# Performance work log

Measured on AMD Instinct MI355X. Metric: run time of the kernel, lower is better.

## Reference

```python
import jax, jax.numpy as jnp
import numpy as np

B, T, E, H = 8, 2048, 512, 16
D = E // H  # 32 embeddings per head
LN_EPS = 1e-3  # keras LayerNormalization default epsilon
DECAY = 1.2


def setup_inputs() -> dict:
    key = jax.random.key(0)
    k0, k1, k2 = jax.random.split(key, 3)
    x = jax.random.normal(k0, (B, T, E), dtype=jnp.float32)
    W = jax.random.normal(k1, (E, E), dtype=jnp.float32) * (1.0 / np.sqrt(E))
    b = jnp.zeros((E,), dtype=jnp.float32)
    concept_map = jax.random.normal(k2, (H, D, D, D), dtype=jnp.float32) * 0.02
    gamma = jnp.ones((E,), dtype=jnp.float32)
    beta = jnp.zeros((E,), dtype=jnp.float32)
    return {"x": x, "W": W, "b": b, "concept_map": concept_map,
            "gamma": gamma, "beta": beta}


def reference(x, W, b, concept_map, gamma, beta):
    Bn, Tn, En = x.shape
    Hn = concept_map.shape[0]
    Dn = En // Hn
    # Dense projection, split into heads: (B,T,H,D)
    h = (jnp.einsum('bte,ef->btf', x, W) + b).reshape(Bn, Tn, Hn, Dn)
    # Decayed cumulative sum of preceding tokens: S_0 = 0, S_t = (S_{t-1} + h_{t-1}) / 1.2
    def step(s, h_t):
        return (s + h_t) / DECAY, s
    _, S = jax.lax.scan(step, jnp.zeros((Bn, Hn, Dn), h.dtype),
                        jnp.swapaxes(h, 0, 1))  # S: (T,B,H,D)
    S = jnp.swapaxes(S, 0, 1)  # (B,T,H,D)
    # Fused bilinear contraction: sum_{i,j} h[...,i] * S[...,j] * C[h,k,i,j]
    # (equivalent to outer-product * concept_map then reduce_sum over last two dims)
    y = jnp.einsum('bthi,bthj,hkij->bthk', h, S, concept_map) + h
    y = y.reshape(Bn, Tn, En)
    # LayerNormalization over last axis (keras default eps=1e-3)
    mu = jnp.mean(y, axis=-1, keepdims=True)
    var = jnp.var(y, axis=-1, keepdims=True)
    y = (y - mu) * jax.lax.rsqrt(var + LN_EPS) * gamma + beta
    # Dropout: identity at inference
    return y
```

## Files before the change

### kernel.cpp

```cpp
#include <hip/hip_runtime.h>
#include <hip/hip_bf16.h>

#define Bn 8
#define Tn 2048
#define En 512
#define Hn 16
#define Dn 32
#define NC 32
#define CL 64
#define NT (Bn*Tn)
#define INV_DECAY (1.0f/1.2f)
#define LOG2_INVD (-0.26303440583379383f)

typedef __attribute__((ext_vector_type(8))) short  bf16x8;
typedef __attribute__((ext_vector_type(4))) float  f32x4;
typedef __attribute__((ext_vector_type(8))) unsigned short u16x8;

__device__ __forceinline__ unsigned short f2b(float f) {
    __hip_bfloat16 h = __float2bfloat16(f);
    return *reinterpret_cast<unsigned short*>(&h);
}
__device__ __forceinline__ float b2f(unsigned short u) {
    union { unsigned int i; float f; } c; c.i = ((unsigned int)u) << 16; return c.f;
}

__host__ __device__ constexpr float wpow(int e) {
    float r = 1.f;
    for (int i = 0; i < e; i++) r *= (1.0f / 1.2f);
    return r;
}

__device__ __forceinline__ size_t hm(int hd, int tok, int ch) {
    return (size_t)hd * ((size_t)NT * Dn) + (size_t)tok * Dn + ch;
}

__global__ __launch_bounds__(256) void prep_k(const float* __restrict__ C,
                                              unsigned short* __restrict__ Cl,
                                              const float* __restrict__ W,
                                              unsigned short* __restrict__ Wt) {
    __shared__ float tile[32][33];
    if (blockIdx.x < 256) {
        const int g = blockIdx.x * 256 + threadIdx.x;
        const int hd = g >> 12, rem = g & 4095;
        const int i = rem >> 7, half = (rem >> 6) & 1, lane = rem & 63;
        const int tloc = lane & 15, kgrp = lane >> 4;
        const int k = half * 16 + tloc;
        const float* src = C + (size_t)hd * 32768 + (size_t)k * 1024 + i * 32 + kgrp * 8;
        float4 a = reinterpret_cast<const float4*>(src)[0];
        float4 b = reinterpret_cast<const float4*>(src)[1];
        u16x8 st;
        st[0]=f2b(a.x); st[1]=f2b(a.y); st[2]=f2b(a.z); st[3]=f2b(a.w);
        st[4]=f2b(b.x); st[5]=f2b(b.y); st[6]=f2b(b.z); st[7]=f2b(b.w);
        *reinterpret_cast<u16x8*>(Cl + (size_t)g * 8) = st;
    } else {
        const int bid = blockIdx.x - 256;
        const int kb = (bid & 15) * 32, nb = (bid >> 4) * 32;
        const int tx = threadIdx.x & 31, ty = threadIdx.x >> 5;
        #pragma unroll
        for (int j = 0; j < 4; j++)
            tile[ty + 8 * j][tx] = W[(size_t)(kb + ty + 8 * j) * En + nb + tx];
        __syncthreads();
        #pragma unroll
        for (int j = 0; j < 4; j++)
            Wt[(size_t)(nb + ty + 8 * j) * En + kb + tx] = f2b(tile[tx][ty + 8 * j]);
    }
}

__global__ __launch_bounds__(256) void gemm_mfma_k(const float* __restrict__ x,
                                                   const unsigned short* __restrict__ Wt,
                                                   const float* __restrict__ bias,
                                                   unsigned short* __restrict__ h,
                                                   float* __restrict__ locals) {
    __shared__ unsigned short As[128][40];
    __shared__ unsigned short Bs[64][40];
    const int m0 = blockIdx.x * 128, n0 = blockIdx.y * 64;
    const int tid = threadIdx.x;
    const int wid = tid >> 6, lane = tid & 63;
    const int tloc = lane & 15, kgrp = lane >> 4;
    const int wr = wid >> 1, wc = wid & 1;

    const int ar = tid >> 1, ah = (tid & 1) * 16;
    const int brr = tid >> 2, bq = (tid & 3) * 8;

    f32x4 acc[4][2] = {};

    for (int k0 = 0; k0 < En; k0 += 32) {
        const float* xp = &x[(size_t)(m0 + ar) * En + k0 + ah];
        float4 a0 = reinterpret_cast<const float4*>(xp)[0];
        float4 a1 = reinterpret_cast<const float4*>(xp)[1];
        float4 a2 = reinterpret_cast<const float4*>(xp)[2];
        float4 a3 = reinterpret_cast<const float4*>(xp)[3];
        u16x8 bv = *reinterpret_cast<const u16x8*>(&Wt[(size_t)(n0 + brr) * En + k0 + bq]);
        __syncthreads();
        u16x8 w0, w1;
        w0[0]=f2b(a0.x); w0[1]=f2b(a0.y); w0[2]=f2b(a0.z); w0[3]=f2b(a0.w);
        w0[4]=f2b(a1.x); w0[5]=f2b(a1.y); w0[6]=f2b(a1.z); w0[7]=f2b(a1.w);
        w1[0]=f2b(a2.x); w1[1]=f2b(a2.y); w1[2]=f2b(a2.z); w1[3]=f2b(a2.w);
        w1[4]=f2b(a3.x); w1[5]=f2b(a3.y); w1[6]=f2b(a3.z); w1[7]=f2b(a3.w);
        *reinterpret_cast<u16x8*>(&As[ar][ah])     = w0;
        *reinterpret_cast<u16x8*>(&As[ar][ah + 8]) = w1;
        *reinterpret_cast<u16x8*>(&Bs[brr][bq])    = bv;
        __syncthreads();

        bf16x8 afr[4], bfr[2];
        #pragma unroll
        for (int m = 0; m < 4; m++)
            afr[m] = *reinterpret_cast<const bf16x8*>(&As[wr * 64 + m * 16 + tloc][kgrp * 8]);
        #pragma unroll
        for (int n = 0; n < 2; n++)
            bfr[n] = *reinterpret_cast<const bf16x8*>(&Bs[wc * 32 + n * 16 + tloc][kgrp * 8]);
        #pragma unroll
        for (int m = 0; m < 4; m++)
            #pragma unroll
            for (int n = 0; n < 2; n++)
                acc[m][n] = __builtin_amdgcn_mfma_f32_16x16x32_bf16(afr[m], bfr[n], acc[m][n], 0, 0, 0);
    }

    const float kmul = (kgrp & 1 ? 2.0736f : 1.f) * (kgrp & 2 ? 4.29981696f : 1.f);
    const int cg = blockIdx.x * 2 + wr;

    #pragma unroll
    for (int n = 0; n < 2; n++) {
        const int col = n0 + wc * 32 + n * 16 + tloc;
        const float bcol = bias[col];
        const int hd = col >> 5, ch = col & 31;
        float part = 0.f;
        #pragma unroll
        for (int m = 0; m < 4; m++)
            #pragma unroll
            for (int r = 0; r < 4; r++) {
                const int row = m0 + wr * 64 + m * 16 + kgrp * 4 + r;
                const unsigned short hb16 = f2b(acc[m][n][r] + bcol);
                h[hm(hd, row, ch)] = hb16;
                part += b2f(hb16) * (wpow(64 - m * 16 - r) * kmul);
            }
        part += __shfl_xor(part, 16);
        part += __shfl_xor(part, 32);
        if (kgrp == 0) locals[(size_t)cg * En + col] = part;
    }
}

__global__ __launch_bounds__(512) void scan_prefix_k(const float* __restrict__ locals,
                                                     float* __restrict__ Acar) {
    const int b = blockIdx.x;
    const int e = threadIdx.x;
    float invRL = 1.f;
    #pragma unroll
    for (int i = 0; i < CL; i++) invRL *= INV_DECAY;
    float A = 0.f;
    for (int c = 0; c < NC; c++) {
        Acar[(size_t)(b * NC + c) * En + e] = A;
        A = A * invRL + locals[(size_t)(b * NC + c) * En + e];
    }
}

__global__ __launch_bounds__(256, 2) void bilinear10_k(const unsigned short* __restrict__ hg,
                                                       const float* __restrict__ Acar,
                                                       unsigned short* __restrict__ yb,
                                                       const unsigned short* __restrict__ Cl) {
    __shared__ unsigned short hs[64][40];
    __shared__ unsigned short Ss[64][40];
    __shared__ float ys[4][64][33];

    const int hd = blockIdx.y;
    const int cg = blockIdx.x;
    const int tokens0 = cg * 64;
    const int tid = threadIdx.x;
    const int wid = tid >> 6, lane = tid & 63;
    const int tloc = lane & 15, kgrp = lane >> 4;
    const int j0 = kgrp * 8;
    const int c0 = wid * 8;

    bf16x8 afr[8][2];
    {
        const unsigned short* cb = Cl + (size_t)hd * 32768;
        #pragma unroll
        for (int s = 0; s < 8; s++) {
            const int i = wid * 8 + s;
            #pragma unroll
            for (int mt = 0; mt < 2; mt++)
                afr[s][mt] = *reinterpret_cast<const bf16x8*>(
                    cb + ((size_t)((i * 2 + mt) * 64 + lane) * 8));
        }
    }

    float Ac[8];
    #pragma unroll
    for (int e = 0; e < 8; e++)
        Ac[e] = Acar[(size_t)cg * En + hd * Dn + c0 + e];

    {
        const int tok = tid >> 2, c8 = (tid & 3) * 8;
        *reinterpret_cast<u16x8*>(&hs[tok][c8]) =
            *reinterpret_cast<const u16x8*>(hg + hm(hd, tokens0 + tok, c8));
    }
    __syncthreads();

    {
        float P[8];
        u16x8 hv = *reinterpret_cast<const u16x8*>(&hs[lane][c0]);
        #pragma unroll
        for (int e = 0; e < 8; e++) P[e] = b2f(hv[e]);
        #pragma unroll
        for (int k = 0; k < 6; k++) {
            const int dlt = 1 << k;
            const float wk = wpow(1 << k);
            #pragma unroll
            for (int e = 0; e < 8; e++) {
                float o = __shfl_up(P[e], dlt, 64);
                P[e] += (lane >= dlt) ? wk * o : 0.f;
            }
        }
        const float dt = exp2f((float)lane * LOG2_INVD);
        u16x8 sst;
        #pragma unroll
        for (int e = 0; e < 8; e++) {
            float pm1 = __shfl_up(P[e], 1, 64);
            if (lane == 0) pm1 = 0.f;
            sst[e] = f2b(Ac[e] * dt + INV_DECAY * pm1);
        }
        *reinterpret_cast<u16x8*>(&Ss[lane][c0]) = sst;
    }
    __syncthreads();

    u16x8 hreg[4];
    float sf[4][8];
    #pragma unroll
    for (int nt = 0; nt < 4; nt++) {
        const int trow = nt * 16 + tloc;
        hreg[nt] = *reinterpret_cast<const u16x8*>(&hs[trow][c0]);
        u16x8 sv = *reinterpret_cast<const u16x8*>(&Ss[trow][j0]);
        #pragma unroll
        for (int e = 0; e < 8; e++) sf[nt][e] = b2f(sv[e]);
    }

    f32x4 acc[2][4] = {};
    #pragma unroll
    for (int s = 0; s < 8; s++) {
        #pragma unroll
        for (int nt = 0; nt < 4; nt++) {
            const float hsc = b2f(hreg[nt][s]);
            bf16x8 bfrag;
            #pragma unroll
            for (int e = 0; e < 8; e++) bfrag[e] = (short)f2b(hsc * sf[nt][e]);
            acc[0][nt] = __builtin_amdgcn_mfma_f32_16x16x32_bf16(afr[s][0], bfrag, acc[0][nt], 0, 0, 0);
            acc[1][nt] = __builtin_amdgcn_mfma_f32_16x16x32_bf16(afr[s][1], bfrag, acc[1][nt], 0, 0, 0);
        }
    }

    #pragma unroll
    for (int mt = 0; mt < 2; mt++)
        #pragma unroll
        for (int nt = 0; nt < 4; nt++)
            #pragma unroll
            for (int r = 0; r < 4; r++)
                ys[wid][nt * 16 + tloc][mt * 16 + kgrp * 4 + r] = acc[mt][nt][r];
    __syncthreads();

    {
        const int token = tid >> 2, q = tid & 3;
        float y[8];
        #pragma unroll
        for (int e = 0; e < 8; e++) y[e] = 0.f;
        #pragma unroll
        for (int w = 0; w < 4; w++) {
            #pragma unroll
            for (int e = 0; e < 8; e++) y[e] += ys[w][token][q * 8 + e];
        }
        u16x8 hres = *reinterpret_cast<const u16x8*>(&hs[token][q * 8]);
        u16x8 st;
        #pragma unroll
        for (int e = 0; e < 8; e++) st[e] = f2b(y[e] + b2f(hres[e]));
        *reinterpret_cast<u16x8*>(yb + hm(hd, tokens0 + token, q * 8)) = st;
    }
}

__global__ __launch_bounds__(256) void ln_k(const unsigned short* __restrict__ y,
                                            const float* __restrict__ gamma,
                                            const float* __restrict__ beta,
                                            float* __restrict__ out) {
    const int row = blockIdx.x * 4 + (threadIdx.x >> 6);
    const int lane = threadIdx.x & 63;
    u16x8 v = *reinterpret_cast<const u16x8*>(y + hm(lane >> 2, row, (lane & 3) * 8));
    float f[8];
    float s = 0.f, s2 = 0.f;
    #pragma unroll
    for (int e = 0; e < 8; e++) {
        f[e] = b2f(v[e]);
        s += f[e]; s2 += f[e] * f[e];
    }
    #pragma unroll
    for (int off = 1; off < 64; off <<= 1) {
        s  += __shfl_xor(s, off);
        s2 += __shfl_xor(s2, off);
    }
    const float mu = s * (1.f / En);
    const float var = s2 * (1.f / En) - mu * mu;
    const float rs = rsqrtf(var + 1e-3f);
    const int cbase = lane * 8;
    float4 g0 = reinterpret_cast<const float4*>(&gamma[cbase])[0];
    float4 g1 = reinterpret_cast<const float4*>(&gamma[cbase])[1];
    float4 b0 = reinterpret_cast<const float4*>(&beta[cbase])[0];
    float4 b1 = reinterpret_cast<const float4*>(&beta[cbase])[1];
    float4 o0, o1;
    o0.x = (f[0] - mu) * rs * g0.x + b0.x; o0.y = (f[1] - mu) * rs * g0.y + b0.y;
    o0.z = (f[2] - mu) * rs * g0.z + b0.z; o0.w = (f[3] - mu) * rs * g0.w + b0.w;
    o1.x = (f[4] - mu) * rs * g1.x + b1.x; o1.y = (f[5] - mu) * rs * g1.y + b1.y;
    o1.z = (f[6] - mu) * rs * g1.z + b1.z; o1.w = (f[7] - mu) * rs * g1.w + b1.w;
    float* op = out + (size_t)row * En;
    reinterpret_cast<float4*>(op)[lane * 2]     = o0;
    reinterpret_cast<float4*>(op)[lane * 2 + 1] = o1;
}

extern "C" void kernel_launch(void* const* d_in, const int* in_sizes, int n_in,
                              void* d_out, int out_size, void* d_ws, size_t ws_size,
                              hipStream_t stream) {
    const float* x     = (const float*)d_in[0];
    const float* W     = (const float*)d_in[1];
    const float* bias  = (const float*)d_in[2];
    const float* C     = (const float*)d_in[3];
    const float* gamma = (const float*)d_in[4];
    const float* beta  = (const float*)d_in[5];
    float* out = (float*)d_out;

    unsigned short* hb  = (unsigned short*)d_ws;
    unsigned short* yb  = hb + (size_t)Hn * NT * Dn;
    unsigned short* Cl  = yb + (size_t)Hn * NT * Dn;
    unsigned short* Wt  = Cl + (size_t)Hn * Dn * Dn * Dn;
    float* locals = (float*)(Wt + (size_t)En * En);
    float* Acar   = locals + (size_t)Bn * NC * En;

    prep_k<<<512, 256, 0, stream>>>(C, Cl, W, Wt);
    gemm_mfma_k<<<dim3(NT / 128, En / 64), 256, 0, stream>>>(x, Wt, bias, hb, locals);
    scan_prefix_k<<<Bn, 512, 0, stream>>>(locals, Acar);
    bilinear10_k<<<dim3(NT / CL, Hn), 256, 0, stream>>>(hb, Acar, yb, Cl);
    ln_k<<<NT / 4, 256, 0, stream>>>(yb, gamma, beta, out);
}
```

Measured before the change: 81.80 us.

## Fuse chunk-carry prefix scan into bilinear kernel and halve cross-wave reduction buffer

Drops the separate scan_prefix_k launch. Each bilinear block now computes its own carry-in by summing the decayed locals of all preceding chunks in its batch, which means redundant work that grows with the chunk index. The cross-wave reduction now uses a smaller two-slot shared buffer with vectorized f32x4 accumulation, paying for it with an extra barrier. The launch-bounds occupancy hint is raised from 2 to 4, which may force register pressure or spills given the large afr fragment arrays.

New measurement: 104.0 us. 1.27x slower.

```diff
diff --git a/kernel.cpp b/kernel.cpp
--- a/kernel.cpp
+++ b/kernel.cpp
@@ -140,36 +140,24 @@
     }
 }
 
-__global__ __launch_bounds__(512) void scan_prefix_k(const float* __restrict__ locals,
-                                                     float* __restrict__ Acar) {
-    const int b = blockIdx.x;
-    const int e = threadIdx.x;
-    float invRL = 1.f;
-    #pragma unroll
-    for (int i = 0; i < CL; i++) invRL *= INV_DECAY;
-    float A = 0.f;
-    for (int c = 0; c < NC; c++) {
-        Acar[(size_t)(b * NC + c) * En + e] = A;
-        A = A * invRL + locals[(size_t)(b * NC + c) * En + e];
-    }
-}
-
-__global__ __launch_bounds__(256, 2) void bilinear10_k(const unsigned short* __restrict__ hg,
-                                                       const float* __restrict__ Acar,
+__global__ __launch_bounds__(256, 4) void bilinear13_k(const unsigned short* __restrict__ hg,
+                                                       const float* __restrict__ locals,
                                                        unsigned short* __restrict__ yb,
                                                        const unsigned short* __restrict__ Cl) {
     __shared__ unsigned short hs[64][40];
     __shared__ unsigned short Ss[64][40];
-    __shared__ float ys[4][64][33];
+    __shared__ float ys2[2][64][36];
 
     const int hd = blockIdx.y;
     const int cg = blockIdx.x;
+    const int b = cg >> 5, c = cg & 31;
     const int tokens0 = cg * 64;
     const int tid = threadIdx.x;
     const int wid = tid >> 6, lane = tid & 63;
     const int tloc = lane & 15, kgrp = lane >> 4;
     const int j0 = kgrp * 8;
     const int c0 = wid * 8;
+    constexpr float INVRL = wpow(64);
 
     bf16x8 afr[8][2];
     {
@@ -184,15 +172,23 @@
         }
     }
 
-    float Ac[8];
-    #pragma unroll
-    for (int e = 0; e < 8; e++)
-        Ac[e] = Acar[(size_t)cg * En + hd * Dn + c0 + e];
-
     {
         const int tok = tid >> 2, c8 = (tid & 3) * 8;
         *reinterpret_cast<u16x8*>(&hs[tok][c8]) =
             *reinterpret_cast<const u16x8*>(hg + hm(hd, tokens0 + tok, c8));
+    }
+
+    float Ac[8] = {0.f,0.f,0.f,0.f,0.f,0.f,0.f,0.f};
+    {
+        float w = 1.f;
+        for (int cp = c - 1; cp >= 0; --cp) {
+            const float* lp = &locals[(size_t)(b * NC + cp) * En + hd * Dn + c0];
+            float4 l0 = reinterpret_cast<const float4*>(lp)[0];
+            float4 l1 = reinterpret_cast<const float4*>(lp)[1];
+            Ac[0] += w * l0.x; Ac[1] += w * l0.y; Ac[2] += w * l0.z; Ac[3] += w * l0.w;
+            Ac[4] += w * l1.x; Ac[5] += w * l1.y; Ac[6] += w * l1.z; Ac[7] += w * l1.w;
+            w *= INVRL;
+        }
     }
     __syncthreads();
 
@@ -248,29 +244,39 @@
         }
     }
 
-    #pragma unroll
-    for (int mt = 0; mt < 2; mt++)
-        #pragma unroll
-        for (int nt = 0; nt < 4; nt++)
-            #pragma unroll
-            for (int r = 0; r < 4; r++)
-                ys[wid][nt * 16 + tloc][mt * 16 + kgrp * 4 + r] = acc[mt][nt][r];
+    const int ws = wid & 1;
+    if (wid < 2) {
+        #pragma unroll
+        for (int mt = 0; mt < 2; mt++)
+            #pragma unroll
+            for (int nt = 0; nt < 4; nt++)
+                *reinterpret_cast<f32x4*>(&ys2[ws][nt * 16 + tloc][mt * 16 + kgrp * 4]) = acc[mt][nt];
+    }
     __syncthreads();
+    if (wid >= 2) {
+        #pragma unroll
+        for (int mt = 0; mt < 2; mt++)
+            #pragma unroll
+            for (int nt = 0; nt < 4; nt++) {
+                f32x4* p = reinterpret_cast<f32x4*>(&ys2[ws][nt * 16 + tloc][mt * 16 + kgrp * 4]);
+                *p += acc[mt][nt];
+            }
+    }
+    __syncthreads();
 
     {
         const int token = tid >> 2, q = tid & 3;
-        float y[8];
-        #pragma unroll
-        for (int e = 0; e < 8; e++) y[e] = 0.f;
-        #pragma unroll
-        for (int w = 0; w < 4; w++) {
-            #pragma unroll
-            for (int e = 0; e < 8; e++) y[e] += ys[w][token][q * 8 + e];
-        }
+        const f32x4* s0 = reinterpret_cast<const f32x4*>(&ys2[0][token][q * 8]);
+        const f32x4* s1 = reinterpret_cast<const f32x4*>(&ys2[1][token][q * 8]);
+        f32x4 y0 = s0[0] + s1[0];
+        f32x4 y1 = s0[1] + s1[1];
         u16x8 hres = *reinterpret_cast<const u16x8*>(&hs[token][q * 8]);
         u16x8 st;
         #pragma unroll
-        for (int e = 0; e < 8; e++) st[e] = f2b(y[e] + b2f(hres[e]));
+        for (int e = 0; e < 4; e++) {
+            st[e]     = f2b(y0[e] + b2f(hres[e]));
+            st[4 + e] = f2b(y1[e] + b2f(hres[4 + e]));
+        }
         *reinterpret_cast<u16x8*>(yb + hm(hd, tokens0 + token, q * 8)) = st;
     }
 }
@@ -324,15 +330,13 @@
     float* out = (float*)d_out;
 
     unsigned short* hb  = (unsigned short*)d_ws;
-    unsigned short* yb  = hb + (size_t)Hn * NT * Dn;
-    unsigned short* Cl  = yb + (size_t)Hn * NT * Dn;
+    unsigned short* Sg  = hb + (size_t)Hn * NT * Dn;
+    unsigned short* Cl  = Sg + (size_t)Hn * NT * Dn;
     unsigned short* Wt  = Cl + (size_t)Hn * Dn * Dn * Dn;
     float* locals = (float*)(Wt + (size_t)En * En);
-    float* Acar   = locals + (size_t)Bn * NC * En;
 
     prep_k<<<512, 256, 0, stream>>>(C, Cl, W, Wt);
     gemm_mfma_k<<<dim3(NT / 128, En / 64), 256, 0, stream>>>(x, Wt, bias, hb, locals);
-    scan_prefix_k<<<Bn, 512, 0, stream>>>(locals, Acar);
-    bilinear10_k<<<dim3(NT / CL, Hn), 256, 0, stream>>>(hb, Acar, yb, Cl);
-    ln_k<<<NT / 4, 256, 0, stream>>>(yb, gamma, beta, out);
-}
+    bilinear13_k<<<dim3(NT / CL, Hn), 256, 0, stream>>>(hb, locals, Sg, Cl);
+    ln_k<<<NT / 4, 256, 0, stream>>>(Sg, gamma, beta, out);
+}
```
